# Kernel optimization log

Hardware: AMD Instinct MI355X
Metric: run time of the kernel (lower is better)

## Reference

```python
import jax, jax.numpy as jnp
import numpy as np

N_NODES = 50000
N_EDGES = 800000
HEADS = 8
CH = 64


def setup_inputs() -> dict:
    key = jax.random.key(0)
    ks = jax.random.split(key, 30)
    rn = lambda k, shape, s=0.1: (jax.random.normal(k, shape, jnp.float32) * s)
    inp = {
        'x': jax.random.normal(ks[0], (N_NODES, 3), jnp.float32),
        'edge_index': jax.random.randint(ks[1], (2, N_EDGES), 0, N_NODES, jnp.int32),
        'edge_attr': jax.random.normal(ks[2], (N_EDGES, 1), jnp.float32),
        'return_attention_weights': 1,
        # node / residual encoders
        'Wn': rn(ks[3], (3, 64)), 'bn': jnp.zeros((64,), jnp.float32),
        'Wr': rn(ks[4], (3, 512)), 'br': jnp.zeros((512,), jnp.float32),
        'W1': rn(ks[5], (64, 512)), 'as1': rn(ks[6], (HEADS, CH)), 'ad1': rn(ks[7], (HEADS, CH)), 'bc1': jnp.zeros((512,), jnp.float32),
        'W2': rn(ks[8], (512, 512)), 'as2': rn(ks[9], (HEADS, CH)), 'ad2': rn(ks[10], (HEADS, CH)), 'bc2': jnp.zeros((512,), jnp.float32),
        'W3': rn(ks[11], (512, 512)), 'as3': rn(ks[12], (HEADS, CH)), 'ad3': rn(ks[13], (HEADS, CH)), 'bc3': jnp.zeros((64,), jnp.float32),
        # node head
        'Wo': rn(ks[14], (64, 2)), 'bo': jnp.zeros((2,), jnp.float32),
        # edge classifier MLP 136 -> 256 -> 2
        'Wm1': rn(ks[15], (136, 256)), 'bm1': jnp.zeros((256,), jnp.float32),
        'Wm2': rn(ks[16], (256, 2)), 'bm2': jnp.zeros((2,), jnp.float32),
    }
    return inp


def _gat(h, src, dst, W, a_src, a_dst, b, concat):
    """PyG GATConv (shared lin, edge_dim=None, eval-mode dropout)."""
    n = h.shape[0]
    g = (h @ W).reshape(n, HEADS, CH)                      # [N,H,C]
    asrc = jnp.sum(g * a_src[None], -1)                    # [N,H]
    adst = jnp.sum(g * a_dst[None], -1)                    # [N,H]
    e = jax.nn.leaky_relu(asrc[src] + adst[dst], 0.2)      # [E',H]
    m = jax.ops.segment_max(e, dst, num_segments=n)        # softmax per destination
    ex = jnp.exp(e - m[dst])
    s = jax.ops.segment_sum(ex, dst, num_segments=n)
    alpha = ex / s[dst]                                    # [E',H]
    out = jax.ops.segment_sum(g[src] * alpha[..., None], dst, num_segments=n)  # [N,H,C]
    out = out.reshape(n, HEADS * CH) if concat else out.mean(axis=1)
    return out + b, alpha


def reference(x, edge_index, edge_attr, return_attention_weights,
              Wn, bn, Wr, br,
              W1, as1, ad1, bc1,
              W2, as2, ad2, bc2,
              W3, as3, ad3, bc3,
              Wo, bo, Wm1, bm1, Wm2, bm2):
    n = x.shape[0]
    e_len = edge_attr.shape[0]
    src0, dst0 = edge_index[0], edge_index[1]
    # GATConv adds self loops internally
    loop = jnp.arange(n, dtype=edge_index.dtype)
    src = jnp.concatenate([src0, loop])
    dst = jnp.concatenate([dst0, loop])

    h = x @ Wn + bn          # node_encoder (dropout is eval identity)
    res = x @ Wr + br        # self.linear residual
    # edge_encoder output is unused by GATConv (edge_dim=None) -> no-op

    o, _ = _gat(h, src, dst, W1, as1, ad1, bc1, concat=True)
    o = jax.nn.elu(o) + res
    o, _ = _gat(o, src, dst, W2, as2, ad2, bc2, concat=True)
    o = jax.nn.elu(o) + res
    o, alpha = _gat(o, src, dst, W3, as3, ad3, bc3, concat=False)
    node_embedding = jax.nn.elu(o)                          # [N,64]

    x_out = node_embedding @ Wo + bo                        # [N,2]
    edge_embedding = jnp.concatenate(
        [node_embedding[src0], alpha[:e_len], node_embedding[dst0]], axis=-1)  # [E,136]
    edge_out = jax.nn.relu(edge_embedding @ Wm1 + bm1) @ Wm2 + bm2             # [E,2]
    return x_out, edge_out
```

## Files before the change

kernel.cpp:

```cpp
#include <hip/hip_runtime.h>
#include <hip/hip_bf16.h>
#include <math.h>

#define N_NODES 50000
#define NPAD    50048
#define N_EDGES 800000
#define EPRIME  (N_EDGES + N_NODES)
#define HEADS 8
#define CH 64
#define FDIM 512

typedef unsigned short ushort_t;
typedef __attribute__((ext_vector_type(8))) short bf16x8_t;
typedef __attribute__((ext_vector_type(4))) float f32x4_t;
typedef __attribute__((ext_vector_type(2))) float f32x2_t;

__device__ __forceinline__ float bf2f(unsigned short u) {
  union { unsigned int i; float f; } v; v.i = ((unsigned int)u) << 16; return v.f;
}
__device__ __forceinline__ unsigned short f2bf(float f) {
  union { float f; unsigned int i; } v; v.f = f;
  unsigned int x = v.i;
  return (unsigned short)((x + 0x7fffu + ((x >> 16) & 1u)) >> 16);
}
__device__ __forceinline__ float ldf(const void* p, size_t idx, int isf32) {
  return isf32 ? ((const float*)p)[idx] : bf2f(((const ushort_t*)p)[idx]);
}
__device__ __forceinline__ void stf(void* p, size_t idx, float v, int isf32) {
  if (isf32) ((float*)p)[idx] = v;
  else       ((ushort_t*)p)[idx] = f2bf(v);
}
__device__ __forceinline__ float leakyf(float v) { return v >= 0.f ? v : 0.2f * v; }
__device__ __forceinline__ float eluf(float v)   { return v > 0.f ? v : expm1f(v); }

__device__ __forceinline__ f32x2_t sp2(float s) { return (f32x2_t){s, s}; }
__device__ __forceinline__ f32x2_t bfpair(unsigned int u) {
  union { unsigned int i; float f; } lo, hi;
  lo.i = u << 16; hi.i = u & 0xffff0000u;
  return (f32x2_t){lo.f, hi.f};
}

__device__ __forceinline__ float dpp_sum64(float x) {
  x += __int_as_float(__builtin_amdgcn_update_dpp(0, __float_as_int(x), 0xB1, 0xf, 0xf, false));
  x += __int_as_float(__builtin_amdgcn_update_dpp(0, __float_as_int(x), 0x4E, 0xf, 0xf, false));
  x += __int_as_float(__builtin_amdgcn_update_dpp(0, __float_as_int(x), 0x141, 0xf, 0xf, false));
  x += __int_as_float(__builtin_amdgcn_update_dpp(0, __float_as_int(x), 0x140, 0xf, 0xf, false));
  x += __int_as_float(__builtin_amdgcn_update_dpp(0, __float_as_int(x), 0x142, 0xa, 0xf, false));
  x += __int_as_float(__builtin_amdgcn_update_dpp(0, __float_as_int(x), 0x143, 0xc, 0xf, false));
  return x;
}

typedef const __attribute__((address_space(1))) unsigned int* gas1_t;
typedef __attribute__((address_space(3))) unsigned int* las3_t;
__device__ __forceinline__ void gll16(const ushort_t* g, ushort_t* l) {
  __builtin_amdgcn_global_load_lds((gas1_t)g, (las3_t)l, 16, 0, 0);
}

__global__ void detect_dtype(const void* Wn, int* flag) {
  const ushort_t* u = (const ushort_t*)Wn;
  int lane = threadIdx.x;
  int cnt = 0;
  for (int i = lane; i < 384; i += 64) {
    float v = fabsf(bf2f(u[i]));
    if (v != 0.f && (v > 16.f || v < 6.1e-5f)) cnt++;
  }
  #pragma unroll
  for (int off = 32; off > 0; off >>= 1) cnt += __shfl_down(cnt, off);
  if (lane == 0) *flag = (cnt >= 20) ? 1 : 0;
}

__global__ __launch_bounds__(256) void convert_wt_t(const void* __restrict__ src,
                                                    ushort_t* __restrict__ dst,
                                                    int K, int N, int boff,
                                                    const int* __restrict__ dflag) {
  int isf32 = *dflag;
  __shared__ float tile[32][33];
  int n0 = blockIdx.x * 32, k0 = blockIdx.y * 32;
  int tx = threadIdx.x & 31, ty = threadIdx.x >> 5;
  #pragma unroll
  for (int r = 0; r < 4; ++r)
    tile[ty + 8 * r][tx] = ldf(src, (size_t)(boff + k0 + ty + 8 * r) * N + n0 + tx, isf32);
  __syncthreads();
  #pragma unroll
  for (int r = 0; r < 4; ++r)
    dst[(size_t)(n0 + ty + 8 * r) * K + k0 + tx] = f2bf(tile[tx][ty + 8 * r]);
}

__global__ void convert_att(const void* s1, const void* d1, const void* s2, const void* d2,
                            const void* s3, const void* d3, ushort_t* __restrict__ dst,
                            const int* __restrict__ dflag) {
  int isf32 = *dflag;
  int tid = blockIdx.x * blockDim.x + threadIdx.x;
  if (tid >= 6 * 512) return;
  int which = tid >> 9, idx = tid & 511;
  const void* p = which == 0 ? s1 : which == 1 ? d1 : which == 2 ? s2
                : which == 3 ? d2 : which == 4 ? s3 : d3;
  dst[tid] = f2bf(ldf(p, idx, isf32));
}

__global__ void init_deg(int* deg, int* fill) {
  int n = blockIdx.x * blockDim.x + threadIdx.x;
  if (n < N_NODES) { deg[n] = 1; fill[n] = 0; }
}

__global__ void count_edges(const int* __restrict__ ei, int* deg) {
  int e = blockIdx.x * blockDim.x + threadIdx.x;
  if (e < N_EDGES) atomicAdd(&deg[ei[N_EDGES + e]], 1);
}

__global__ __launch_bounds__(1024) void scan1024(const int* __restrict__ deg,
                                                 int* __restrict__ rowptr) {
  const int CHUNK = (N_NODES + 1023) / 1024;
  int t = threadIdx.x;
  int wave = t >> 6, lane = t & 63;
  int lo = t * CHUNK;
  int hi = lo + CHUNK; if (hi > N_NODES) hi = N_NODES;
  int s = 0;
  for (int i = lo; i < hi; ++i) s += deg[i];
  int inc = s;
  #pragma unroll
  for (int off = 1; off < 64; off <<= 1) {
    int u = __shfl_up(inc, off);
    if (lane >= off) inc += u;
  }
  __shared__ int wsum[16];
  if (lane == 63) wsum[wave] = inc;
  __syncthreads();
  int wbase = 0;
  for (int w = 0; w < wave; ++w) wbase += wsum[w];
  int run = wbase + inc - s;
  for (int i = lo; i < hi; ++i) { rowptr[i] = run; run += deg[i]; }
  if (t == 1023) rowptr[N_NODES] = run;
}

__global__ void fill_csr(const int* __restrict__ ei, const int* __restrict__ rowptr,
                         int* fill, int* __restrict__ csr_src) {
  int e = blockIdx.x * blockDim.x + threadIdx.x;
  if (e >= EPRIME) return;
  int s, d;
  if (e < N_EDGES) { s = ei[e]; d = ei[N_EDGES + e]; }
  else             { s = d = e - N_EDGES; }
  int pos = rowptr[d] + atomicAdd(&fill[d], 1);
  csr_src[pos] = s;
}

__global__ void encode_h(const void* __restrict__ x, const void* __restrict__ Wn,
                         const void* __restrict__ bn, ushort_t* __restrict__ h,
                         const int* __restrict__ dflag) {
  int isf32 = *dflag;
  int tid = blockIdx.x * blockDim.x + threadIdx.x;
  if (tid >= N_NODES * 64) return;
  int n = tid >> 6, j = tid & 63;
  float x0 = ldf(x, n * 3 + 0, isf32), x1 = ldf(x, n * 3 + 1, isf32), x2 = ldf(x, n * 3 + 2, isf32);
  float v = x0 * ldf(Wn, j, isf32) + x1 * ldf(Wn, 64 + j, isf32)
          + x2 * ldf(Wn, 128 + j, isf32) + ldf(bn, j, isf32);
  h[tid] = f2bf(v);
}

__global__ __launch_bounds__(256) void gemm_bt(
    const ushort_t* __restrict__ A, const ushort_t* __restrict__ BT,
    ushort_t* __restrict__ C, int K, int ldc,
    const ushort_t* __restrict__ att, float* __restrict__ asrc, float* __restrict__ adst)
{
  __shared__ __align__(16) ushort_t As[128][32];
  __shared__ __align__(16) ushort_t Bs[128][32];
  int tid = threadIdx.x;
  int wave = tid >> 6, lane = tid & 63;
  int wr = wave >> 1, wc = wave & 1;
  int row0 = blockIdx.x * 128, col0 = blockIdx.y * 128;
  int fm = lane & 15, fq = lane >> 4;

  f32x4_t acc[4][4];
  #pragma unroll
  for (int i = 0; i < 4; ++i)
    #pragma unroll
    for (int j = 0; j < 4; ++j) acc[i][j] = (f32x4_t){0.f, 0.f, 0.f, 0.f};

  int srow = wave * 32 + (lane >> 2);
  int skel = (lane & 3) * 8;
  const ushort_t* aG0 = A  + (size_t)(row0 + srow) * K + skel;
  const ushort_t* aG1 = A  + (size_t)(row0 + srow + 16) * K + skel;
  const ushort_t* bG0 = BT + (size_t)(col0 + srow) * K + skel;
  const ushort_t* bG1 = BT + (size_t)(col0 + srow + 16) * K + skel;
  ushort_t* aL0 = &As[wave * 32][0];
  ushort_t* aL1 = &As[wave * 32 + 16][0];
  ushort_t* bL0 = &Bs[wave * 32][0];
  ushort_t* bL1 = &Bs[wave * 32 + 16][0];

  for (int k0 = 0; k0 < K; k0 += 32) {
    gll16(aG0 + k0, aL0);
    gll16(aG1 + k0, aL1);
    gll16(bG0 + k0, bL0);
    gll16(bG1 + k0, bL1);
    __syncthreads();
    bf16x8_t af[4], bfr[4];
    #pragma unroll
    for (int i = 0; i < 4; ++i) af[i]  = *(const bf16x8_t*)&As[64 * wr + 16 * i + fm][fq * 8];
    #pragma unroll
    for (int j = 0; j < 4; ++j) bfr[j] = *(const bf16x8_t*)&Bs[64 * wc + 16 * j + fm][fq * 8];
    #pragma unroll
    for (int i = 0; i < 4; ++i)
      #pragma unroll
      for (int j = 0; j < 4; ++j)
        acc[i][j] = __builtin_amdgcn_mfma_f32_16x16x32_bf16(af[i], bfr[j], acc[i][j], 0, 0, 0);
    __syncthreads();
  }

  int do_att = (att != nullptr);
  int head = 2 * blockIdx.y + wc;
  float sa[4], sd[4];
  if (do_att) {
    #pragma unroll
    for (int j = 0; j < 4; ++j) {
      int ch = 16 * j + fm;
      sa[j] = bf2f(att[head * CH + ch]);
      sd[j] = bf2f(att[512 + head * CH + ch]);
    }
  }

  #pragma unroll
  for (int i = 0; i < 4; ++i) {
    int rowb = row0 + 64 * wr + 16 * i + fq * 4;
    #pragma unroll
    for (int r = 0; r < 4; ++r) {
      int row = rowb + r;
      float ss = 0.f, dd = 0.f;
      #pragma unroll
      for (int j = 0; j < 4; ++j) {
        ushort_t uv = f2bf(acc[i][j][r]);
        C[(size_t)row * ldc + col0 + 64 * wc + 16 * j + fm] = uv;
        if (do_att) {
          float cv = bf2f(uv);
          ss += cv * sa[j];
          dd += cv * sd[j];
        }
      }
      if (do_att) {
        #pragma unroll
        for (int off = 8; off > 0; off >>= 1) {
          ss += __shfl_down(ss, off);
          dd += __shfl_down(dd, off);
        }
        if (fm == 0 && row < N_NODES) {
          asrc[row * HEADS + head] = ss;
          adst[row * HEADS + head] = dd;
        }
      }
    }
  }
}

__global__ __launch_bounds__(256) void aggregate2(
    const int* __restrict__ rowptr, const int* __restrict__ csr_src,
    const float* __restrict__ asrc, const float* __restrict__ adst,
    float* __restrict__ sumv,
    const ushort_t* __restrict__ g,
    const void* __restrict__ x, const void* __restrict__ Wr,
    const void* __restrict__ br, const void* __restrict__ bc,
    ushort_t* __restrict__ out, int mean_mode,
    const void* __restrict__ Wo, const void* __restrict__ bo,
    void* __restrict__ outh, const int* __restrict__ dflag)
{
  int isf32 = *dflag;
  __shared__ float red[4][512];
  __shared__ float lred[4][8];
  __shared__ float sx[3];
  int n = blockIdx.x;
  int t = threadIdx.x;
  int wave = t >> 6, lane = t & 63;
  if (t < 3) sx[t] = ldf(x, n * 3 + t, isf32);

  int ch0 = lane * 8;
  int hh  = lane >> 3;
  int start = rowptr[n], end = rowptr[n + 1];
  float ad = adst[n * HEADS + hh];

  f32x2_t acc2[4];
  #pragma unroll
  for (int k = 0; k < 4; ++k) acc2[k] = (f32x2_t){0.f, 0.f};
  float l = 0.f;

  int i = start + wave;
  for (; i + 4 < end; i += 8) {
    int iu0 = __builtin_amdgcn_readfirstlane(i);
    int iu1 = __builtin_amdgcn_readfirstlane(i + 4);
    int s0 = csr_src[iu0];
    int s1 = csr_src[iu1];
    float e0 = asrc[s0 * HEADS + hh] + ad;
    float e1 = asrc[s1 * HEADS + hh] + ad;
    uint4 gv0 = *(const uint4*)(g + (size_t)s0 * FDIM + ch0);
    uint4 gv1 = *(const uint4*)(g + (size_t)s1 * FDIM + ch0);
    float p0 = __expf(leakyf(e0));
    float p1 = __expf(leakyf(e1));
    l += p0 + p1;
    f32x2_t q0 = sp2(p0), q1 = sp2(p1);
    acc2[0] += q0 * bfpair(gv0.x); acc2[0] += q1 * bfpair(gv1.x);
    acc2[1] += q0 * bfpair(gv0.y); acc2[1] += q1 * bfpair(gv1.y);
    acc2[2] += q0 * bfpair(gv0.z); acc2[2] += q1 * bfpair(gv1.z);
    acc2[3] += q0 * bfpair(gv0.w); acc2[3] += q1 * bfpair(gv1.w);
  }
  if (i < end) {
    int iu0 = __builtin_amdgcn_readfirstlane(i);
    int s0 = csr_src[iu0];
    float e0 = asrc[s0 * HEADS + hh] + ad;
    uint4 gv0 = *(const uint4*)(g + (size_t)s0 * FDIM + ch0);
    float p0 = __expf(leakyf(e0));
    l += p0;
    f32x2_t q0 = sp2(p0);
    acc2[0] += q0 * bfpair(gv0.x);
    acc2[1] += q0 * bfpair(gv0.y);
    acc2[2] += q0 * bfpair(gv0.z);
    acc2[3] += q0 * bfpair(gv0.w);
  }

  #pragma unroll
  for (int k = 0; k < 4; ++k) {
    red[wave][ch0 + 2 * k]     = acc2[k][0];
    red[wave][ch0 + 2 * k + 1] = acc2[k][1];
  }
  if ((lane & 7) == 0) lred[wave][hh] = l;
  __syncthreads();

  int c0 = t * 2;
  int h  = t >> 5;
  float a0 = red[0][c0]     + red[1][c0]     + red[2][c0]     + red[3][c0];
  float a1 = red[0][c0 + 1] + red[1][c0 + 1] + red[2][c0 + 1] + red[3][c0 + 1];
  float lt = lred[0][h] + lred[1][h] + lred[2][h] + lred[3][h];
  a0 /= lt;
  a1 /= lt;
  if ((t & 31) == 0) sumv[n * HEADS + h] = 1.f / lt;

  if (!mean_mode) {
    float r0 = sx[0] * ldf(Wr, c0, isf32)         + sx[1] * ldf(Wr, 512 + c0, isf32)
             + sx[2] * ldf(Wr, 1024 + c0, isf32)  + ldf(br, c0, isf32);
    float r1 = sx[0] * ldf(Wr, c0 + 1, isf32)     + sx[1] * ldf(Wr, 512 + c0 + 1, isf32)
             + sx[2] * ldf(Wr, 1024 + c0 + 1, isf32) + ldf(br, c0 + 1, isf32);
    unsigned int o0 = f2bf(eluf(a0 + ldf(bc, c0, isf32)) + r0);
    unsigned int o1 = f2bf(eluf(a1 + ldf(bc, c0 + 1, isf32)) + r1);
    *(unsigned int*)(out + (size_t)n * FDIM + c0) = o0 | (o1 << 16);
  } else {
    __syncthreads();
    red[0][c0] = a0; red[0][c0 + 1] = a1;
    __syncthreads();
    if (t < 64) {
      float tot = 0.f;
      #pragma unroll
      for (int hh2 = 0; hh2 < 8; ++hh2) tot += red[0][t + 64 * hh2];
      ushort_t uv = f2bf(eluf(tot * 0.125f + ldf(bc, t, isf32)));
      out[(size_t)n * CH + t] = uv;
      float nv = bf2f(uv);
      float p0 = nv * ldf(Wo, t * 2 + 0, isf32);
      float p1 = nv * ldf(Wo, t * 2 + 1, isf32);
      float vv = (t & 1) ? p1 : p0;
      float ww = (t & 1) ? p0 : p1;
      vv += __shfl_xor(ww, 1);
      #pragma unroll
      for (int off = 2; off < 64; off <<= 1) vv += __shfl_xor(vv, off);
      if (t < 2) stf(outh, (size_t)n * 2 + t, vv + ldf(bo, t, isf32), isf32);
    }
  }
}

#define EPW 32
__global__ __launch_bounds__(256) void edge_head8(
    const int* __restrict__ ei, const float* __restrict__ asrc, const float* __restrict__ adst,
    const float* __restrict__ rsumv,
    const ushort_t* __restrict__ pq, const void* __restrict__ Wm1,
    const void* __restrict__ bm1, const void* __restrict__ Wm2,
    const void* __restrict__ bm2, void* __restrict__ out,
    const int* __restrict__ dflag)
{
  int isf32 = *dflag;
  int lane = threadIdx.x & 63;
  int c0 = lane * 4;
  int h = lane & 7;
  f32x2_t w1r[8][2], w2a[2], w2b[2], b1r[2];
  #pragma unroll
  for (int hh = 0; hh < 8; ++hh)
    #pragma unroll
    for (int jp = 0; jp < 2; ++jp)
      w1r[hh][jp] = (f32x2_t){ ldf(Wm1, (64 + hh) * 256 + c0 + 2 * jp, isf32),
                               ldf(Wm1, (64 + hh) * 256 + c0 + 2 * jp + 1, isf32) };
  #pragma unroll
  for (int jp = 0; jp < 2; ++jp) {
    w2a[jp] = (f32x2_t){ ldf(Wm2, (c0 + 2 * jp) * 2 + 0, isf32),
                         ldf(Wm2, (c0 + 2 * jp + 1) * 2 + 0, isf32) };
    w2b[jp] = (f32x2_t){ ldf(Wm2, (c0 + 2 * jp) * 2 + 1, isf32),
                         ldf(Wm2, (c0 + 2 * jp + 1) * 2 + 1, isf32) };
    b1r[jp] = (f32x2_t){ ldf(bm1, c0 + 2 * jp, isf32),
                         ldf(bm1, c0 + 2 * jp + 1, isf32) };
  }
  float bo0 = ldf(bm2, 0, isf32), bo1 = ldf(bm2, 1, isf32);
  const f32x2_t zero2 = (f32x2_t){0.f, 0.f};

  int wid = blockIdx.x * 4 + (threadIdx.x >> 6);
  int e0 = wid * EPW;

  float vA, vB, rsA, rsB;
  uint2 pvA, qvA, pvB, qvB;
  {
    int eu = __builtin_amdgcn_readfirstlane(e0);
    int sA = ei[eu],     dA = ei[N_EDGES + eu];
    int sB = ei[eu + 1], dB = ei[N_EDGES + eu + 1];
    vA = asrc[sA * HEADS + h] + adst[dA * HEADS + h];
    vB = asrc[sB * HEADS + h] + adst[dB * HEADS + h];
    rsA = rsumv[dA * HEADS + h]; rsB = rsumv[dB * HEADS + h];
    pvA = *(const uint2*)(pq + (size_t)sA * FDIM + c0);
    qvA = *(const uint2*)(pq + (size_t)dA * FDIM + 256 + c0);
    pvB = *(const uint2*)(pq + (size_t)sB * FDIM + c0);
    qvB = *(const uint2*)(pq + (size_t)dB * FDIM + 256 + c0);
  }

  #pragma unroll
  for (int it = 0; it < EPW / 2; ++it) {
    int e = e0 + 2 * it;
    float cvA = vA, cvB = vB, crsA = rsA, crsB = rsB;
    uint2 cpvA = pvA, cqvA = qvA, cpvB = pvB, cqvB = qvB;
    if (it + 1 < EPW / 2) {
      int eu = __builtin_amdgcn_readfirstlane(e + 2);
      int sA = ei[eu],     dA = ei[N_EDGES + eu];
      int sB = ei[eu + 1], dB = ei[N_EDGES + eu + 1];
      vA = asrc[sA * HEADS + h] + adst[dA * HEADS + h];
      vB = asrc[sB * HEADS + h] + adst[dB * HEADS + h];
      rsA = rsumv[dA * HEADS + h]; rsB = rsumv[dB * HEADS + h];
      pvA = *(const uint2*)(pq + (size_t)sA * FDIM + c0);
      qvA = *(const uint2*)(pq + (size_t)dA * FDIM + 256 + c0);
      pvB = *(const uint2*)(pq + (size_t)sB * FDIM + c0);
      qvB = *(const uint2*)(pq + (size_t)dB * FDIM + 256 + c0);
    }

    float aA = __expf(leakyf(cvA)) * crsA;
    float aB = __expf(leakyf(cvB)) * crsB;
    float alA[8], alB[8];
    #pragma unroll
    for (int hh = 0; hh < 8; ++hh) {
      alA[hh] = __int_as_float(__builtin_amdgcn_readlane(__float_as_int(aA), hh));
      alB[hh] = __int_as_float(__builtin_amdgcn_readlane(__float_as_int(aB), hh));
    }

    f32x2_t pA2[2] = { bfpair(cpvA.x), bfpair(cpvA.y) };
    f32x2_t qA2[2] = { bfpair(cqvA.x), bfpair(cqvA.y) };
    f32x2_t pB2[2] = { bfpair(cpvB.x), bfpair(cpvB.y) };
    f32x2_t qB2[2] = { bfpair(cqvB.x), bfpair(cqvB.y) };
    f32x2_t aA0 = zero2, aA1 = zero2, aB0 = zero2, aB1 = zero2;
    #pragma unroll
    for (int jp = 0; jp < 2; ++jp) {
      f32x2_t hvA = pA2[jp] + qA2[jp] + b1r[jp];
      f32x2_t hvB = pB2[jp] + qB2[jp] + b1r[jp];
      #pragma unroll
      for (int hh = 0; hh < 8; ++hh) {
        hvA += sp2(alA[hh]) * w1r[hh][jp];
        hvB += sp2(alB[hh]) * w1r[hh][jp];
      }
      hvA = __builtin_elementwise_max(hvA, zero2);
      hvB = __builtin_elementwise_max(hvB, zero2);
      aA0 += hvA * w2a[jp]; aA1 += hvA * w2b[jp];
      aB0 += hvB * w2a[jp]; aB1 += hvB * w2b[jp];
    }
    float accA0 = aA0[0] + aA0[1];
    float accA1 = aA1[0] + aA1[1];
    float accB0 = aB0[0] + aB0[1];
    float accB1 = aB1[0] + aB1[1];
    accA0 = dpp_sum64(accA0);
    accA1 = dpp_sum64(accA1);
    accB0 = dpp_sum64(accB0);
    accB1 = dpp_sum64(accB1);
    if (lane == 63) {
      stf(out, 100000 + (size_t)e * 2 + 0, accA0 + bo0, isf32);
      stf(out, 100000 + (size_t)e * 2 + 1, accA1 + bo1, isf32);
      stf(out, 100000 + (size_t)e * 2 + 2, accB0 + bo0, isf32);
      stf(out, 100000 + (size_t)e * 2 + 3, accB1 + bo1, isf32);
    }
  }
}

extern "C" void kernel_launch(void* const* d_in, const int* in_sizes, int n_in,
                              void* d_out, int out_size, void* d_ws, size_t ws_size,
                              hipStream_t stream) {
  const void* x   = d_in[0];
  const int*  ei  = (const int*)d_in[1];
  const void* Wn  = d_in[4];
  const void* bn  = d_in[5];
  const void* Wr  = d_in[6];
  const void* br  = d_in[7];
  const void* W1  = d_in[8];
  const void* as1 = d_in[9];
  const void* ad1 = d_in[10];
  const void* bc1 = d_in[11];
  const void* W2  = d_in[12];
  const void* as2 = d_in[13];
  const void* ad2 = d_in[14];
  const void* bc2 = d_in[15];
  const void* W3  = d_in[16];
  const void* as3 = d_in[17];
  const void* ad3 = d_in[18];
  const void* bc3 = d_in[19];
  const void* Wo  = d_in[20];
  const void* bo  = d_in[21];
  const void* Wm1 = d_in[22];
  const void* bm1 = d_in[23];
  const void* Wm2 = d_in[24];
  const void* bm2 = d_in[25];

  char* ws = (char*)d_ws;
  size_t off = 0;
  auto take = [&](size_t bytes) -> char* {
    char* p = ws + off;
    off += (bytes + 255) & ~(size_t)255;
    return p;
  };
  ushort_t* h_bf   = (ushort_t*)take((size_t)NPAD * 64 * 2);
  ushort_t* g_bf   = (ushort_t*)take((size_t)NPAD * FDIM * 2);
  ushort_t* o_bf   = (ushort_t*)take((size_t)NPAD * FDIM * 2);
  float*    asrc   = (float*)take((size_t)N_NODES * HEADS * 4);
  float*    adst   = (float*)take((size_t)N_NODES * HEADS * 4);
  float*    sumv   = (float*)take((size_t)N_NODES * HEADS * 4);
  int*      rowptr = (int*)take((size_t)(N_NODES + 1) * 4);
  int*      csr_src= (int*)take((size_t)EPRIME * 4);
  int*      deg    = (int*)take((size_t)N_NODES * 4);
  int*      fillc  = (int*)take((size_t)N_NODES * 4);
  int*      dflag  = (int*)take(256);
  ushort_t* WT1    = (ushort_t*)take((size_t)512 * 64 * 2);
  ushort_t* WT2    = (ushort_t*)take((size_t)512 * 512 * 2);
  ushort_t* WT3    = (ushort_t*)take((size_t)512 * 512 * 2);
  ushort_t* WTPQ   = (ushort_t*)take((size_t)512 * 64 * 2);
  ushort_t* attv   = (ushort_t*)take((size_t)6 * 512 * 2);

  dim3 b256(256);
  const int MB = NPAD / 128;

  detect_dtype<<<dim3(1), dim3(64), 0, stream>>>(Wn, dflag);

  convert_wt_t<<<dim3(16, 2),  b256, 0, stream>>>(W1, WT1, 64, 512, 0, dflag);
  convert_wt_t<<<dim3(16, 16), b256, 0, stream>>>(W2, WT2, 512, 512, 0, dflag);
  convert_wt_t<<<dim3(16, 16), b256, 0, stream>>>(W3, WT3, 512, 512, 0, dflag);
  convert_wt_t<<<dim3(8, 2),   b256, 0, stream>>>(Wm1, WTPQ,            64, 256, 0,  dflag);
  convert_wt_t<<<dim3(8, 2),   b256, 0, stream>>>(Wm1, WTPQ + 256 * 64, 64, 256, 72, dflag);
  convert_att<<<dim3(12),  b256, 0, stream>>>(as1, ad1, as2, ad2, as3, ad3, attv, dflag);

  init_deg<<<dim3((N_NODES + 255) / 256), b256, 0, stream>>>(deg, fillc);
  count_edges<<<dim3((N_EDGES + 255) / 256), b256, 0, stream>>>(ei, deg);
  scan1024<<<dim3(1), dim3(1024), 0, stream>>>(deg, rowptr);
  fill_csr<<<dim3((EPRIME + 255) / 256), b256, 0, stream>>>(ei, rowptr, fillc, csr_src);

  encode_h<<<dim3((N_NODES * 64 + 255) / 256), b256, 0, stream>>>(x, Wn, bn, h_bf, dflag);

  gemm_bt<<<dim3(MB, 4), b256, 0, stream>>>(h_bf, WT1, g_bf, 64, 512,
                                            attv, asrc, adst);
  aggregate2<<<dim3(N_NODES), b256, 0, stream>>>(rowptr, csr_src, asrc, adst, sumv,
                                                 g_bf, x, Wr, br, bc1, o_bf, 0,
                                                 nullptr, nullptr, d_out, dflag);

  gemm_bt<<<dim3(MB, 4), b256, 0, stream>>>(o_bf, WT2, g_bf, 512, 512,
                                            attv + 1024, asrc, adst);
  aggregate2<<<dim3(N_NODES), b256, 0, stream>>>(rowptr, csr_src, asrc, adst, sumv,
                                                 g_bf, x, Wr, br, bc2, o_bf, 0,
                                                 nullptr, nullptr, d_out, dflag);

  gemm_bt<<<dim3(MB, 4), b256, 0, stream>>>(o_bf, WT3, g_bf, 512, 512,
                                            attv + 2048, asrc, adst);
  aggregate2<<<dim3(N_NODES), b256, 0, stream>>>(rowptr, csr_src, asrc, adst, sumv,
                                                 g_bf, x, Wr, br, bc3, h_bf, 1,
                                                 Wo, bo, d_out, dflag);

  gemm_bt<<<dim3(MB, 4), b256, 0, stream>>>(h_bf, WTPQ, g_bf, 64, 512,
                                            nullptr, nullptr, nullptr);
  edge_head8<<<dim3(N_EDGES / (EPW * 4)), b256, 0, stream>>>(ei, asrc, adst, sumv, g_bf,
                                                             Wm1, bm1, Wm2, bm2,
                                                             d_out, dflag);
}
```

Before: 1.016 ms.

## Reorder layer-1 GAT to aggregate 64-dim inputs before block-diagonal projection

```diff
diff --git a/kernel.cpp b/kernel.cpp
--- a/kernel.cpp
+++ b/kernel.cpp
@@ -96,6 +96,165 @@
   const void* p = which == 0 ? s1 : which == 1 ? d1 : which == 2 ? s2
                 : which == 3 ? d2 : which == 4 ? s3 : d3;
   dst[tid] = f2bf(ldf(p, idx, isf32));
+}
+
+__global__ void att_w1(const void* __restrict__ W1, const void* __restrict__ as1,
+                       const void* __restrict__ ad1, float* __restrict__ wt_att,
+                       const int* __restrict__ dflag) {
+  int isf32 = *dflag;
+  int t = blockIdx.x * blockDim.x + threadIdx.x;
+  if (t >= 64 * 16) return;
+  int c = t >> 4, q = t & 15, head = q >> 1, sd = q & 1;
+  const void* a = sd ? ad1 : as1;
+  float s = 0.f;
+  for (int ch = 0; ch < 64; ++ch)
+    s += ldf(W1, (size_t)c * 512 + head * 64 + ch, isf32) * ldf(a, head * 64 + ch, isf32);
+  wt_att[t] = s;
+}
+
+__global__ __launch_bounds__(256) void coef1(const ushort_t* __restrict__ h,
+                                             const float* __restrict__ wt_att,
+                                             float* __restrict__ asrc,
+                                             float* __restrict__ adst) {
+  __shared__ float sh[16][64];
+  __shared__ float sw[64][16];
+  int t = threadIdx.x;
+  int nb = blockIdx.x * 16;
+  #pragma unroll
+  for (int r = 0; r < 4; ++r) {
+    int idx = t + 256 * r;
+    sh[idx >> 6][idx & 63] = bf2f(h[(size_t)nb * 64 + idx]);
+    sw[idx >> 4][idx & 15] = wt_att[idx];
+  }
+  __syncthreads();
+  int node = t >> 4, q = t & 15;
+  float s = 0.f;
+  #pragma unroll
+  for (int c = 0; c < 64; ++c) s += sh[node][c] * sw[c][q];
+  int n = nb + node, head = q >> 1;
+  if (q & 1) adst[n * 8 + head] = s;
+  else       asrc[n * 8 + head] = s;
+}
+
+__global__ __launch_bounds__(256) void aggregate_h(
+    const int* __restrict__ rowptr, const int* __restrict__ csr_src,
+    const float* __restrict__ asrc, const float* __restrict__ adst,
+    const ushort_t* __restrict__ h, ushort_t* __restrict__ agg)
+{
+  __shared__ float red[4][8][64];
+  __shared__ float lred[4][8];
+  int n = blockIdx.x;
+  int t = threadIdx.x;
+  int wave = t >> 6, lane = t & 63;
+  int start = rowptr[n], end = rowptr[n + 1];
+  const float4* adp = (const float4*)(adst + n * 8);
+  float4 ad0 = adp[0], ad1v = adp[1];
+  float accv[8], lv[8];
+  #pragma unroll
+  for (int k2 = 0; k2 < 8; ++k2) { accv[k2] = 0.f; lv[k2] = 0.f; }
+
+  for (int i = start + wave; i < end; i += 4) {
+    int iu = __builtin_amdgcn_readfirstlane(i);
+    int s = csr_src[iu];
+    float hv = bf2f(h[(size_t)s * 64 + lane]);
+    const float4* ap = (const float4*)(asrc + s * 8);
+    float4 a0 = ap[0], a1 = ap[1];
+    float al[8];
+    al[0] = __expf(leakyf(a0.x + ad0.x));
+    al[1] = __expf(leakyf(a0.y + ad0.y));
+    al[2] = __expf(leakyf(a0.z + ad0.z));
+    al[3] = __expf(leakyf(a0.w + ad0.w));
+    al[4] = __expf(leakyf(a1.x + ad1v.x));
+    al[5] = __expf(leakyf(a1.y + ad1v.y));
+    al[6] = __expf(leakyf(a1.z + ad1v.z));
+    al[7] = __expf(leakyf(a1.w + ad1v.w));
+    #pragma unroll
+    for (int k2 = 0; k2 < 8; ++k2) { accv[k2] += al[k2] * hv; lv[k2] += al[k2]; }
+  }
+
+  #pragma unroll
+  for (int k2 = 0; k2 < 8; ++k2) red[wave][k2][lane] = accv[k2];
+  if (lane == 0) {
+    #pragma unroll
+    for (int k2 = 0; k2 < 8; ++k2) lred[wave][k2] = lv[k2];
+  }
+  __syncthreads();
+  int hh = t >> 5, c0 = (t & 31) * 2;
+  float l = lred[0][hh] + lred[1][hh] + lred[2][hh] + lred[3][hh];
+  float rl = 1.f / l;
+  float v0 = (red[0][hh][c0]     + red[1][hh][c0]     + red[2][hh][c0]     + red[3][hh][c0])     * rl;
+  float v1 = (red[0][hh][c0 + 1] + red[1][hh][c0 + 1] + red[2][hh][c0 + 1] + red[3][hh][c0 + 1]) * rl;
+  unsigned int o = (unsigned int)f2bf(v0) | ((unsigned int)f2bf(v1) << 16);
+  *(unsigned int*)(agg + (size_t)n * FDIM + hh * 64 + c0) = o;
+}
+
+__global__ __launch_bounds__(256) void gemm_bd(
+    const ushort_t* __restrict__ agg, const ushort_t* __restrict__ BT,
+    ushort_t* __restrict__ o,
+    const void* __restrict__ x, const void* __restrict__ Wr,
+    const void* __restrict__ br, const void* __restrict__ bc,
+    const int* __restrict__ dflag)
+{
+  int isf32 = *dflag;
+  int tid = threadIdx.x;
+  int wave = tid >> 6, lane = tid & 63;
+  int wr_ = wave >> 1, wc = wave & 1;
+  int row0 = blockIdx.x * 128, col0 = blockIdx.y * 128;
+  int fm = lane & 15, fq = lane >> 4;
+
+  f32x4_t acc[4][4];
+  #pragma unroll
+  for (int i = 0; i < 4; ++i)
+    #pragma unroll
+    for (int j = 0; j < 4; ++j) acc[i][j] = (f32x4_t){0.f, 0.f, 0.f, 0.f};
+
+  #pragma unroll
+  for (int ks = 0; ks < 2; ++ks) {
+    bf16x8_t af[4], bfr[4];
+    #pragma unroll
+    for (int i = 0; i < 4; ++i)
+      af[i] = *(const bf16x8_t*)(agg + (size_t)(row0 + 64 * wr_ + 16 * i + fm) * FDIM
+                                     + col0 + 64 * wc + ks * 32 + fq * 8);
+    #pragma unroll
+    for (int j = 0; j < 4; ++j)
+      bfr[j] = *(const bf16x8_t*)(BT + (size_t)(col0 + 64 * wc + 16 * j + fm) * 64
+                                     + ks * 32 + fq * 8);
+    #pragma unroll
+    for (int i = 0; i < 4; ++i)
+      #pragma unroll
+      for (int j = 0; j < 4; ++j)
+        acc[i][j] = __builtin_amdgcn_mfma_f32_16x16x32_bf16(af[i], bfr[j], acc[i][j], 0, 0, 0);
+  }
+
+  float wra[4], wrb[4], wrc[4], bb[4], brr[4];
+  #pragma unroll
+  for (int j = 0; j < 4; ++j) {
+    int col = col0 + 64 * wc + 16 * j + fm;
+    wra[j] = ldf(Wr, col, isf32);
+    wrb[j] = ldf(Wr, 512 + col, isf32);
+    wrc[j] = ldf(Wr, 1024 + col, isf32);
+    brr[j] = ldf(br, col, isf32);
+    bb[j]  = ldf(bc, col, isf32);
+  }
+  #pragma unroll
+  for (int i = 0; i < 4; ++i) {
+    int rowb = row0 + 64 * wr_ + 16 * i + fq * 4;
+    #pragma unroll
+    for (int r = 0; r < 4; ++r) {
+      int row = rowb + r;
+      if (row < N_NODES) {
+        float x0 = ldf(x, row * 3 + 0, isf32);
+        float x1 = ldf(x, row * 3 + 1, isf32);
+        float x2 = ldf(x, row * 3 + 2, isf32);
+        #pragma unroll
+        for (int j = 0; j < 4; ++j) {
+          float rres = x0 * wra[j] + x1 * wrb[j] + x2 * wrc[j] + brr[j];
+          float v = eluf(acc[i][j][r] + bb[j]) + rres;
+          o[(size_t)row * FDIM + col0 + 64 * wc + 16 * j + fm] = f2bf(v);
+        }
+      }
+    }
+  }
 }
 
 __global__ void init_deg(int* deg, int* fill) {
@@ -525,6 +684,7 @@
   ushort_t* WT3    = (ushort_t*)take((size_t)512 * 512 * 2);
   ushort_t* WTPQ   = (ushort_t*)take((size_t)512 * 64 * 2);
   ushort_t* attv   = (ushort_t*)take((size_t)6 * 512 * 2);
+  float*    wt_att = (float*)take((size_t)64 * 16 * 4);
 
   dim3 b256(256);
   const int MB = NPAD / 128;
@@ -537,6 +697,7 @@
   convert_wt_t<<<dim3(8, 2),   b256, 0, stream>>>(Wm1, WTPQ,            64, 256, 0,  dflag);
   convert_wt_t<<<dim3(8, 2),   b256, 0, stream>>>(Wm1, WTPQ + 256 * 64, 64, 256, 72, dflag);
   convert_att<<<dim3(12),  b256, 0, stream>>>(as1, ad1, as2, ad2, as3, ad3, attv, dflag);
+  att_w1<<<dim3(4), b256, 0, stream>>>(W1, as1, ad1, wt_att, dflag);
 
   init_deg<<<dim3((N_NODES + 255) / 256), b256, 0, stream>>>(deg, fillc);
   count_edges<<<dim3((N_EDGES + 255) / 256), b256, 0, stream>>>(ei, deg);
@@ -545,11 +706,10 @@
 
   encode_h<<<dim3((N_NODES * 64 + 255) / 256), b256, 0, stream>>>(x, Wn, bn, h_bf, dflag);
 
-  gemm_bt<<<dim3(MB, 4), b256, 0, stream>>>(h_bf, WT1, g_bf, 64, 512,
-                                            attv, asrc, adst);
-  aggregate2<<<dim3(N_NODES), b256, 0, stream>>>(rowptr, csr_src, asrc, adst, sumv,
-                                                 g_bf, x, Wr, br, bc1, o_bf, 0,
-                                                 nullptr, nullptr, d_out, dflag);
+  coef1<<<dim3(N_NODES / 16), b256, 0, stream>>>(h_bf, wt_att, asrc, adst);
+  aggregate_h<<<dim3(N_NODES), b256, 0, stream>>>(rowptr, csr_src, asrc, adst,
+                                                  h_bf, g_bf);
+  gemm_bd<<<dim3(MB, 4), b256, 0, stream>>>(g_bf, WT1, o_bf, x, Wr, br, bc1, dflag);
 
   gemm_bt<<<dim3(MB, 4), b256, 0, stream>>>(o_bf, WT2, g_bf, 512, 512,
                                             attv + 1024, asrc, adst);
```

After: 1.050 ms. +3.4%, slower.
